# Kernel optimization log

Measured on AMD Instinct MI355X. Metric: run time of the kernel, lower is better.

## Reference

```python
import jax, jax.numpy as jnp
import numpy as np

B, S, C, V = 8, 256, 256, 64

def setup_inputs() -> dict:
    key = jax.random.key(0)
    ks = jax.random.split(key, 11)
    bound = 1.0 / np.sqrt(C)
    u = lambda k, shape: jax.random.uniform(k, shape, jnp.float32, -bound, bound)
    return {
        "ctx": jax.random.normal(ks[0], (B, S, C), jnp.float32),
        "W": u(ks[1], (C, C, V)),
        "bias": u(ks[2], (V,)),
        "lin1_w": u(ks[3], (V, C)), "lin1_b": u(ks[4], (V,)),
        "lin2_w": u(ks[5], (V, C)), "lin2_b": u(ks[6], (V,)),
        "linmul_w": u(ks[7], (V, C)), "linmul_b": u(ks[8], (V,)),
        "lindiff_w": u(ks[9], (V, C)), "lindiff_b": u(ks[10], (V,)),
    }

def reference(ctx, W, bias, lin1_w, lin1_b, lin2_w, lin2_b,
              linmul_w, linmul_b, lindiff_w, lindiff_b):
    # bilinear: out[b,s,z,k] = sum_ij ctx[b,s,i] * ctx[b,z,j] * W[i,j,k]
    tmp = jnp.einsum('bsi,ijk->bsjk', ctx, W)          # (B,S,C,V)
    out = jnp.einsum('bsjk,bzj->bszk', tmp, ctx)       # (B,S,S,V)
    out = out + bias
    out1 = ctx @ lin1_w.T + lin1_b                     # (B,S,V)
    out2 = ctx @ lin2_w.T + lin2_b                     # (B,S,V)
    # mul[b,s,z] = ctx[b,z] * ctx[b,s]; diff[b,s,z] = ctx[b,z] - ctx[b,s]
    mul = ctx[:, None, :, :] * ctx[:, :, None, :]      # (B,S,S,C)
    diff = ctx[:, None, :, :] - ctx[:, :, None, :]     # (B,S,S,C)
    outmul = mul @ linmul_w.T + linmul_b               # (B,S,S,V)
    outdiff = diff @ lindiff_w.T + lindiff_b           # (B,S,S,V)
    return jnp.tanh(out + out1[:, None, :, :] + out2[:, :, None, :] + outmul + outdiff)
```

## Files before the change

kernel.cpp:

```cpp
#include <hip/hip_runtime.h>


typedef __attribute__((ext_vector_type(8))) _Float16 half8;
typedef __attribute__((ext_vector_type(4))) _Float16 half4v;
typedef __attribute__((ext_vector_type(4))) float f32x4;

__device__ __forceinline__ void async16(const void* g, void* l) {
  __builtin_amdgcn_global_load_lds(
      (__attribute__((address_space(1))) void*)g,
      (__attribute__((address_space(3))) void*)l, 16, 0, 0);
}

__global__ __launch_bounds__(256) void prep_ctx(const float* __restrict__ ctx,
                                                _Float16* __restrict__ ch) {
  int idx = (blockIdx.x * 256 + threadIdx.x) * 4;
  float4 v = *(const float4*)(ctx + idx);
  half4v o;
  o[0] = (_Float16)v.x; o[1] = (_Float16)v.y;
  o[2] = (_Float16)v.z; o[3] = (_Float16)v.w;
  *(half4v*)(ch + idx) = o;
}

__global__ __launch_bounds__(256) void prep_wt(const float* __restrict__ W,
                                               const float* __restrict__ lmw,
                                               _Float16* __restrict__ wt) {
  __shared__ _Float16 T[256 * 68];
  const int t = threadIdx.x;
  const int j = blockIdx.x;
#pragma unroll
  for (int p = 0; p < 16; ++p) {
    int i = p * 16 + (t >> 4);
    int c = t & 15;
    float4 v = *(const float4*)&W[(size_t)i * 16384 + j * 64 + c * 4];
    if (i == j) {
      v.x += lmw[(c * 4 + 0) * 256 + j];
      v.y += lmw[(c * 4 + 1) * 256 + j];
      v.z += lmw[(c * 4 + 2) * 256 + j];
      v.w += lmw[(c * 4 + 3) * 256 + j];
    }
    half4v o;
    o[0] = (_Float16)v.x; o[1] = (_Float16)v.y;
    o[2] = (_Float16)v.z; o[3] = (_Float16)v.w;
    *(half4v*)&T[i * 68 + c * 4] = o;
  }
  __syncthreads();
  const int k = t >> 2, i0 = (t & 3) * 64;
  _Float16* dst = wt + ((size_t)(k * 256 + j)) * 256 + i0;
#pragma unroll
  for (int u = 0; u < 64; u += 8) {
    half8 o;
#pragma unroll
    for (int e = 0; e < 8; ++e) o[e] = T[(i0 + u + e) * 68 + k];
    *(half8*)(dst + u) = o;
  }
}

__global__ __launch_bounds__(256) void prep_rt(
    const float* __restrict__ ctx, const float* __restrict__ bias,
    const float* __restrict__ l1w, const float* __restrict__ l1b,
    const float* __restrict__ l2w, const float* __restrict__ l2b,
    const float* __restrict__ lmb, const float* __restrict__ ldw,
    const float* __restrict__ ldb, float* __restrict__ rbuf,
    float* __restrict__ tbuf) {
  __shared__ float Cs[16 * 256];
  const int t = threadIdx.x;
  const int row0 = blockIdx.x * 16;
#pragma unroll
  for (int p = 0; p < 4; ++p)
    ((float4*)Cs)[p * 256 + t] =
        ((const float4*)(ctx + (size_t)row0 * 256))[p * 256 + t];
  __syncthreads();
  const int k = t & 63, lr = t >> 6;
  const float* l1r = l1w + k * 256;
  const float* l2r = l2w + k * 256;
  const float* ldr = ldw + k * 256;
  float a1[4] = {0.f, 0.f, 0.f, 0.f};
  float a2[4] = {0.f, 0.f, 0.f, 0.f};
  for (int c = 0; c < 256; c += 4) {
    float4 w1 = *(const float4*)(l1r + c);
    float4 w2 = *(const float4*)(l2r + c);
    float4 wd = *(const float4*)(ldr + c);
    float4 s1, s2;
    s1.x = w1.x + wd.x; s1.y = w1.y + wd.y; s1.z = w1.z + wd.z; s1.w = w1.w + wd.w;
    s2.x = w2.x - wd.x; s2.y = w2.y - wd.y; s2.z = w2.z - wd.z; s2.w = w2.w - wd.w;
#pragma unroll
    for (int u = 0; u < 4; ++u) {
      float4 cv = *(const float4*)(&Cs[(lr * 4 + u) * 256 + c]);
      a1[u] += cv.x * s1.x + cv.y * s1.y + cv.z * s1.z + cv.w * s1.w;
      a2[u] += cv.x * s2.x + cv.y * s2.y + cv.z * s2.z + cv.w * s2.w;
    }
  }
  float tb = l2b[k] + bias[k] + lmb[k] + ldb[k];
  float rb = l1b[k];
#pragma unroll
  for (int u = 0; u < 4; ++u) {
    int row = row0 + lr * 4 + u;
    rbuf[row * 64 + k] = a1[u] + rb;
    tbuf[row * 64 + k] = a2[u] + tb;
  }
}

__global__ __launch_bounds__(256) void gemm1(const _Float16* __restrict__ ch,
                                             const _Float16* __restrict__ wt,
                                             _Float16* __restrict__ tmp) {
  __shared__ _Float16 pool[4 * 64 * 72];
  _Float16* As = pool;
  _Float16* Bs = pool + 8192;
  const int t = threadIdx.x;
  const int lane = t & 63, wave = t >> 6;
  const int d = blockIdx.x + blockIdx.y * 128;
  const int w = (d & 7) * 256 + (d >> 3);
  const int m0 = (w & 15) * 128, n0 = (w >> 4) * 128;
  const int wm = (wave & 1) * 64, wn = (wave >> 1) * 64;
  const int r = lane & 15, q = lane >> 4;
  const int sr = r & 7;
  f32x4 acc[4][4] = {};
  const int cg = (t & 7) ^ ((t >> 3) & 7);
  const _Float16* gA = ch + (size_t)(m0 + (t >> 3)) * 256 + cg * 8;
  const _Float16* gB = wt + (size_t)(n0 + (t >> 3)) * 256 + cg * 8;
  for (int k0 = 0; k0 < 256; k0 += 64) {
#pragma unroll
    for (int p = 0; p < 4; ++p) {
      async16(gA + p * 32 * 256 + k0, &As[p * 2048 + t * 8]);
      async16(gB + p * 32 * 256 + k0, &Bs[p * 2048 + t * 8]);
    }
    __syncthreads();
#pragma unroll
    for (int kk = 0; kk < 2; ++kk) {
      const int ca = ((kk * 4 + q) ^ sr) * 8;
      half8 a[4], b[4];
#pragma unroll
      for (int mi = 0; mi < 4; ++mi)
        a[mi] = *(const half8*)&As[(wm + mi * 16 + r) * 64 + ca];
#pragma unroll
      for (int ni = 0; ni < 4; ++ni)
        b[ni] = *(const half8*)&Bs[(wn + ni * 16 + r) * 64 + ca];
#pragma unroll
      for (int ni = 0; ni < 4; ++ni)
#pragma unroll
        for (int mi = 0; mi < 4; ++mi)
          acc[ni][mi] = __builtin_amdgcn_mfma_f32_16x16x32_f16(
              b[ni], a[mi], acc[ni][mi], 0, 0, 0);
    }
    __syncthreads();
  }
  _Float16* Sw = pool + wave * 4608;
#pragma unroll
  for (int ni = 0; ni < 4; ++ni)
#pragma unroll
    for (int mi = 0; mi < 4; ++mi) {
      half4v h;
#pragma unroll
      for (int e = 0; e < 4; ++e) h[e] = (_Float16)acc[ni][mi][e];
      *(half4v*)&Sw[(mi * 16 + r) * 72 + ni * 16 + q * 4] = h;
    }
  __syncthreads();
  const int g2 = lane >> 3, c2 = lane & 7;
  _Float16* dst = tmp + (size_t)(m0 + wm) * 16384 + (n0 + wn);
#pragma unroll
  for (int u = 0; u < 8; ++u) {
    int row = u * 8 + g2;
    half8 vv = *(const half8*)&Sw[row * 72 + c2 * 8];
    *(half8*)(dst + (size_t)row * 16384 + c2 * 8) = vv;
  }
}

__global__ __launch_bounds__(256) void gemm2(const _Float16* __restrict__ ch,
                                             const _Float16* __restrict__ tmp,
                                             const float* __restrict__ rbuf,
                                             const float* __restrict__ tbuf,
                                             float* __restrict__ out) {
  __shared__ _Float16 As[128 * 64];
  __shared__ _Float16 Bs[128 * 64];
  const int t = threadIdx.x;
  const int lane = t & 63, wave = t >> 6;
  const int d = blockIdx.x;
  const int b = d & 7;
  const int idx = d >> 3;
  const int m0 = (idx & 1) * 128;
  const int n0 = (idx >> 1) * 128;
  const int wm = (wave & 1) * 64, wn = (wave >> 1) * 64;
  const int r = lane & 15, q = lane >> 4;
  const int sr = r & 7;
  f32x4 acc[4][4] = {};
  const _Float16* chb = ch + (size_t)b * 65536;
  const _Float16* tmb = tmp + (size_t)b * 4194304;
  const int cg = (t & 7) ^ ((t >> 3) & 7);
  const _Float16* gA = chb + (size_t)(m0 + (t >> 3)) * 256 + cg * 8;
  const _Float16* gB = tmb + (size_t)(n0 + (t >> 3)) * 256 + cg * 8;
  for (int k0 = 0; k0 < 256; k0 += 64) {
#pragma unroll
    for (int p = 0; p < 4; ++p) {
      async16(gA + p * 32 * 256 + k0, &As[p * 2048 + t * 8]);
      async16(gB + p * 32 * 256 + k0, &Bs[p * 2048 + t * 8]);
    }
    __syncthreads();
#pragma unroll
    for (int kk = 0; kk < 2; ++kk) {
      const int ca = ((kk * 4 + q) ^ sr) * 8;
      half8 a[4], bf[4];
#pragma unroll
      for (int mi = 0; mi < 4; ++mi)
        a[mi] = *(const half8*)&As[(wm + mi * 16 + r) * 64 + ca];
#pragma unroll
      for (int ni = 0; ni < 4; ++ni)
        bf[ni] = *(const half8*)&Bs[(wn + ni * 16 + r) * 64 + ca];
#pragma unroll
      for (int ni = 0; ni < 4; ++ni)
#pragma unroll
        for (int mi = 0; mi < 4; ++mi)
          acc[ni][mi] = __builtin_amdgcn_mfma_f32_16x16x32_f16(
              bf[ni], a[mi], acc[ni][mi], 0, 0, 0);
    }
    __syncthreads();
  }
  const int s = (n0 >> 6) + (wn >> 6);
  const float* rb = rbuf + (size_t)b * 16384;
  const float* tb = tbuf + ((size_t)(b * 256 + s)) * 64;
  float* ob = out + (size_t)b * 4194304 + (size_t)s * 16384;
#pragma unroll
  for (int ni = 0; ni < 4; ++ni)
#pragma unroll
    for (int mi = 0; mi < 4; ++mi) {
      int z = m0 + wm + mi * 16 + r;
      int k0 = ni * 16 + q * 4;
      f32x4 rv = *(const f32x4*)&rb[z * 64 + k0];
      f32x4 tv = *(const f32x4*)&tb[k0];
      f32x4 o;
#pragma unroll
      for (int e = 0; e < 4; ++e) {
        float x = acc[ni][mi][e] + rv[e] + tv[e];
        float ax = fabsf(x);
        float ev = __expf(-2.0f * ax);
        float y = (1.0f - ev) / (1.0f + ev);
        o[e] = copysignf(y, x);
      }
      *(f32x4*)&ob[z * 64 + k0] = o;
    }
}

extern "C" void kernel_launch(void* const* d_in, const int* in_sizes, int n_in,
                              void* d_out, int out_size, void* d_ws, size_t ws_size,
                              hipStream_t stream) {
  const float* ctx  = (const float*)d_in[0];
  const float* W    = (const float*)d_in[1];
  const float* bias = (const float*)d_in[2];
  const float* l1w  = (const float*)d_in[3];
  const float* l1b  = (const float*)d_in[4];
  const float* l2w  = (const float*)d_in[5];
  const float* l2b  = (const float*)d_in[6];
  const float* lmw  = (const float*)d_in[7];
  const float* lmb  = (const float*)d_in[8];
  const float* ldw  = (const float*)d_in[9];
  const float* ldb  = (const float*)d_in[10];
  float* out = (float*)d_out;

  char* ws = (char*)d_ws;
  _Float16* ch  = (_Float16*)ws;
  _Float16* wt  = (_Float16*)(ws + (1u << 20));
  _Float16* tmp = (_Float16*)(ws + (9u << 20));
  float* rbuf = (float*)(ws + (73u << 20));
  float* tbuf = rbuf + 2048 * 64;

  prep_ctx<<<512, 256, 0, stream>>>(ctx, ch);
  prep_wt<<<256, 256, 0, stream>>>(W, lmw, wt);
  prep_rt<<<128, 256, 0, stream>>>(ctx, bias, l1w, l1b, l2w, l2b, lmb, ldw, ldb,
                                   rbuf, tbuf);
  gemm1<<<dim3(128, 16), 256, 0, stream>>>(ch, wt, tmp);
  gemm2<<<2048, 256, 0, stream>>>(ch, tmp, rbuf, tbuf, out);
}
```

Baseline: 250.0 us.

## Double-buffer GEMM K-loop with async prefetch and fuse ctx half conversion into prep_rt

Measured after the change: 255.0 us. No clear change (+2.0%).

```diff
diff --git a/kernel.cpp b/kernel.cpp
--- a/kernel.cpp
+++ b/kernel.cpp
@@ -9,16 +9,6 @@
   __builtin_amdgcn_global_load_lds(
       (__attribute__((address_space(1))) void*)g,
       (__attribute__((address_space(3))) void*)l, 16, 0, 0);
-}
-
-__global__ __launch_bounds__(256) void prep_ctx(const float* __restrict__ ctx,
-                                                _Float16* __restrict__ ch) {
-  int idx = (blockIdx.x * 256 + threadIdx.x) * 4;
-  float4 v = *(const float4*)(ctx + idx);
-  half4v o;
-  o[0] = (_Float16)v.x; o[1] = (_Float16)v.y;
-  o[2] = (_Float16)v.z; o[3] = (_Float16)v.w;
-  *(half4v*)(ch + idx) = o;
 }
 
 __global__ __launch_bounds__(256) void prep_wt(const float* __restrict__ W,
@@ -61,7 +51,7 @@
     const float* __restrict__ l2w, const float* __restrict__ l2b,
     const float* __restrict__ lmb, const float* __restrict__ ldw,
     const float* __restrict__ ldb, float* __restrict__ rbuf,
-    float* __restrict__ tbuf) {
+    float* __restrict__ tbuf, _Float16* __restrict__ ch) {
   __shared__ float Cs[16 * 256];
   const int t = threadIdx.x;
   const int row0 = blockIdx.x * 16;
@@ -70,6 +60,16 @@
     ((float4*)Cs)[p * 256 + t] =
         ((const float4*)(ctx + (size_t)row0 * 256))[p * 256 + t];
   __syncthreads();
+  {
+    half8 h0, h1;
+#pragma unroll
+    for (int e = 0; e < 8; ++e) {
+      h0[e] = (_Float16)Cs[t * 16 + e];
+      h1[e] = (_Float16)Cs[t * 16 + 8 + e];
+    }
+    *(half8*)&ch[(size_t)row0 * 256 + t * 16] = h0;
+    *(half8*)&ch[(size_t)row0 * 256 + t * 16 + 8] = h1;
+  }
   const int k = t & 63, lr = t >> 6;
   const float* l1r = l1w + k * 256;
   const float* l2r = l2w + k * 256;
@@ -104,8 +104,6 @@
                                              const _Float16* __restrict__ wt,
                                              _Float16* __restrict__ tmp) {
   __shared__ _Float16 pool[4 * 64 * 72];
-  _Float16* As = pool;
-  _Float16* Bs = pool + 8192;
   const int t = threadIdx.x;
   const int lane = t & 63, wave = t >> 6;
   const int d = blockIdx.x + blockIdx.y * 128;
@@ -113,37 +111,50 @@
   const int m0 = (w & 15) * 128, n0 = (w >> 4) * 128;
   const int wm = (wave & 1) * 64, wn = (wave >> 1) * 64;
   const int r = lane & 15, q = lane >> 4;
-  const int sr = r & 7;
   f32x4 acc[4][4] = {};
-  const int cg = (t & 7) ^ ((t >> 3) & 7);
-  const _Float16* gA = ch + (size_t)(m0 + (t >> 3)) * 256 + cg * 8;
-  const _Float16* gB = wt + (size_t)(n0 + (t >> 3)) * 256 + cg * 8;
-  for (int k0 = 0; k0 < 256; k0 += 64) {
-#pragma unroll
-    for (int p = 0; p < 4; ++p) {
-      async16(gA + p * 32 * 256 + k0, &As[p * 2048 + t * 8]);
-      async16(gB + p * 32 * 256 + k0, &Bs[p * 2048 + t * 8]);
-    }
-    __syncthreads();
-#pragma unroll
-    for (int kk = 0; kk < 2; ++kk) {
-      const int ca = ((kk * 4 + q) ^ sr) * 8;
-      half8 a[4], b[4];
+  const int cg = (t & 3) ^ ((t >> 3) & 3);
+  const _Float16* gA = ch + (size_t)(m0 + (t >> 2)) * 256 + cg * 8;
+  const _Float16* gB = wt + (size_t)(n0 + (t >> 2)) * 256 + cg * 8;
+#define G1_STAGE(buf, k0)                                      \
+  {                                                            \
+    _Float16* Ab = pool + (buf)*8192;                          \
+    _Float16* Bb = pool + (buf)*8192 + 4096;                   \
+    async16(gA + (k0), &Ab[t * 8]);                            \
+    async16(gA + 64 * 256 + (k0), &Ab[2048 + t * 8]);          \
+    async16(gB + (k0), &Bb[t * 8]);                            \
+    async16(gB + 64 * 256 + (k0), &Bb[2048 + t * 8]);          \
+  }
+  G1_STAGE(0, 0);
+  const int ca = (q ^ ((r >> 1) & 3)) * 8;
+#pragma unroll
+  for (int ks = 0; ks < 8; ++ks) {
+    if (ks < 7) {
+      G1_STAGE((ks + 1) & 1, (ks + 1) * 32);
+      asm volatile("s_waitcnt vmcnt(4)" ::: "memory");
+    } else {
+      asm volatile("s_waitcnt vmcnt(0)" ::: "memory");
+    }
+    asm volatile("s_barrier" ::: "memory");
+    const _Float16* Ab = pool + (ks & 1) * 8192;
+    const _Float16* Bb = Ab + 4096;
+    half8 a[4], b[4];
+#pragma unroll
+    for (int mi = 0; mi < 4; ++mi)
+      a[mi] = *(const half8*)&Ab[(wm + mi * 16 + r) * 32 + ca];
+#pragma unroll
+    for (int ni = 0; ni < 4; ++ni)
+      b[ni] = *(const half8*)&Bb[(wn + ni * 16 + r) * 32 + ca];
+    __builtin_amdgcn_s_setprio(1);
+#pragma unroll
+    for (int ni = 0; ni < 4; ++ni)
 #pragma unroll
       for (int mi = 0; mi < 4; ++mi)
-        a[mi] = *(const half8*)&As[(wm + mi * 16 + r) * 64 + ca];
-#pragma unroll
-      for (int ni = 0; ni < 4; ++ni)
-        b[ni] = *(const half8*)&Bs[(wn + ni * 16 + r) * 64 + ca];
-#pragma unroll
-      for (int ni = 0; ni < 4; ++ni)
-#pragma unroll
-        for (int mi = 0; mi < 4; ++mi)
-          acc[ni][mi] = __builtin_amdgcn_mfma_f32_16x16x32_f16(
-              b[ni], a[mi], acc[ni][mi], 0, 0, 0);
-    }
-    __syncthreads();
-  }
+        acc[ni][mi] = __builtin_amdgcn_mfma_f32_16x16x32_f16(
+            b[ni], a[mi], acc[ni][mi], 0, 0, 0);
+    __builtin_amdgcn_s_setprio(0);
+    asm volatile("s_barrier" ::: "memory");
+  }
+#undef G1_STAGE
   _Float16* Sw = pool + wave * 4608;
 #pragma unroll
   for (int ni = 0; ni < 4; ++ni)
@@ -154,7 +165,6 @@
       for (int e = 0; e < 4; ++e) h[e] = (_Float16)acc[ni][mi][e];
       *(half4v*)&Sw[(mi * 16 + r) * 72 + ni * 16 + q * 4] = h;
     }
-  __syncthreads();
   const int g2 = lane >> 3, c2 = lane & 7;
   _Float16* dst = tmp + (size_t)(m0 + wm) * 16384 + (n0 + wn);
 #pragma unroll
@@ -170,8 +180,7 @@
                                              const float* __restrict__ rbuf,
                                              const float* __restrict__ tbuf,
                                              float* __restrict__ out) {
-  __shared__ _Float16 As[128 * 64];
-  __shared__ _Float16 Bs[128 * 64];
+  __shared__ _Float16 pool[16384];
   const int t = threadIdx.x;
   const int lane = t & 63, wave = t >> 6;
   const int d = blockIdx.x;
@@ -181,39 +190,52 @@
   const int n0 = (idx >> 1) * 128;
   const int wm = (wave & 1) * 64, wn = (wave >> 1) * 64;
   const int r = lane & 15, q = lane >> 4;
-  const int sr = r & 7;
   f32x4 acc[4][4] = {};
   const _Float16* chb = ch + (size_t)b * 65536;
   const _Float16* tmb = tmp + (size_t)b * 4194304;
-  const int cg = (t & 7) ^ ((t >> 3) & 7);
-  const _Float16* gA = chb + (size_t)(m0 + (t >> 3)) * 256 + cg * 8;
-  const _Float16* gB = tmb + (size_t)(n0 + (t >> 3)) * 256 + cg * 8;
-  for (int k0 = 0; k0 < 256; k0 += 64) {
-#pragma unroll
-    for (int p = 0; p < 4; ++p) {
-      async16(gA + p * 32 * 256 + k0, &As[p * 2048 + t * 8]);
-      async16(gB + p * 32 * 256 + k0, &Bs[p * 2048 + t * 8]);
-    }
-    __syncthreads();
-#pragma unroll
-    for (int kk = 0; kk < 2; ++kk) {
-      const int ca = ((kk * 4 + q) ^ sr) * 8;
-      half8 a[4], bf[4];
+  const int cg = (t & 3) ^ ((t >> 3) & 3);
+  const _Float16* gA = chb + (size_t)(m0 + (t >> 2)) * 256 + cg * 8;
+  const _Float16* gB = tmb + (size_t)(n0 + (t >> 2)) * 256 + cg * 8;
+#define G2_STAGE(buf, k0)                                      \
+  {                                                            \
+    _Float16* Ab = pool + (buf)*8192;                          \
+    _Float16* Bb = pool + (buf)*8192 + 4096;                   \
+    async16(gA + (k0), &Ab[t * 8]);                            \
+    async16(gA + 64 * 256 + (k0), &Ab[2048 + t * 8]);          \
+    async16(gB + (k0), &Bb[t * 8]);                            \
+    async16(gB + 64 * 256 + (k0), &Bb[2048 + t * 8]);          \
+  }
+  G2_STAGE(0, 0);
+  const int ca = (q ^ ((r >> 1) & 3)) * 8;
+#pragma unroll
+  for (int ks = 0; ks < 8; ++ks) {
+    if (ks < 7) {
+      G2_STAGE((ks + 1) & 1, (ks + 1) * 32);
+      asm volatile("s_waitcnt vmcnt(4)" ::: "memory");
+    } else {
+      asm volatile("s_waitcnt vmcnt(0)" ::: "memory");
+    }
+    asm volatile("s_barrier" ::: "memory");
+    const _Float16* Ab = pool + (ks & 1) * 8192;
+    const _Float16* Bb = Ab + 4096;
+    half8 a[4], bf[4];
+#pragma unroll
+    for (int mi = 0; mi < 4; ++mi)
+      a[mi] = *(const half8*)&Ab[(wm + mi * 16 + r) * 32 + ca];
+#pragma unroll
+    for (int ni = 0; ni < 4; ++ni)
+      bf[ni] = *(const half8*)&Bb[(wn + ni * 16 + r) * 32 + ca];
+    __builtin_amdgcn_s_setprio(1);
+#pragma unroll
+    for (int ni = 0; ni < 4; ++ni)
 #pragma unroll
       for (int mi = 0; mi < 4; ++mi)
-        a[mi] = *(const half8*)&As[(wm + mi * 16 + r) * 64 + ca];
-#pragma unroll
-      for (int ni = 0; ni < 4; ++ni)
-        bf[ni] = *(const half8*)&Bs[(wn + ni * 16 + r) * 64 + ca];
-#pragma unroll
-      for (int ni = 0; ni < 4; ++ni)
-#pragma unroll
-        for (int mi = 0; mi < 4; ++mi)
-          acc[ni][mi] = __builtin_amdgcn_mfma_f32_16x16x32_f16(
-              bf[ni], a[mi], acc[ni][mi], 0, 0, 0);
-    }
-    __syncthreads();
-  }
+        acc[ni][mi] = __builtin_amdgcn_mfma_f32_16x16x32_f16(
+            bf[ni], a[mi], acc[ni][mi], 0, 0, 0);
+    __builtin_amdgcn_s_setprio(0);
+    asm volatile("s_barrier" ::: "memory");
+  }
+#undef G2_STAGE
   const int s = (n0 >> 6) + (wn >> 6);
   const float* rb = rbuf + (size_t)b * 16384;
   const float* tb = tbuf + ((size_t)(b * 256 + s)) * 64;
@@ -262,10 +284,9 @@
   float* rbuf = (float*)(ws + (73u << 20));
   float* tbuf = rbuf + 2048 * 64;
 
-  prep_ctx<<<512, 256, 0, stream>>>(ctx, ch);
+  prep_rt<<<128, 256, 0, stream>>>(ctx, bias, l1w, l1b, l2w, l2b, lmb, ldw, ldb,
+                                   rbuf, tbuf, ch);
   prep_wt<<<256, 256, 0, stream>>>(W, lmw, wt);
-  prep_rt<<<128, 256, 0, stream>>>(ctx, bias, l1w, l1b, l2w, l2b, lmb, ldw, ldb,
-                                   rbuf, tbuf);
   gemm1<<<dim3(128, 16), 256, 0, stream>>>(ch, wt, tmp);
   gemm2<<<2048, 256, 0, stream>>>(ch, tmp, rbuf, tbuf, out);
 }
```
